# Performance work log

Hardware: AMD Instinct MI355X
Metric: run time of the kernel (lower is better)

## Reference

```python
import jax, jax.numpy as jnp
import numpy as np

N_NODES = 50000
N_EDGES = 800000
D_NODE = 128
D_EDGE = 128
D_HID = 128
D_OUT = 128


def setup_inputs() -> dict:
    key = jax.random.key(0)
    ks = jax.random.split(key, 6)
    d_in = 2 * D_NODE + D_EDGE  # 384
    return {
        "cell_attr": jax.random.normal(ks[0], (N_NODES, D_NODE), dtype=jnp.float32),
        "edge_attr": jax.random.normal(ks[1], (N_EDGES, D_EDGE), dtype=jnp.float32),
        "W1": jax.random.normal(ks[2], (d_in, D_HID), dtype=jnp.float32) * (1.0 / np.sqrt(d_in)),
        "b1": jnp.zeros((D_HID,), dtype=jnp.float32),
        "W2": jax.random.normal(ks[3], (D_HID, D_OUT), dtype=jnp.float32) * (1.0 / np.sqrt(D_HID)),
        "b2": jnp.zeros((D_OUT,), dtype=jnp.float32),
        "edge_index": jax.random.randint(ks[4], (2, N_EDGES), 0, N_NODES, dtype=jnp.int64) if jax.config.jax_enable_x64 else jax.random.randint(ks[4], (2, N_EDGES), 0, N_NODES, dtype=jnp.int32),
    }


def reference(cell_attr, edge_attr, W1, b1, W2, b2, edge_index):
    # Gather sender/receiver node features via edge_index: [E, d_node] each
    senders_attr = cell_attr[edge_index[0]]
    receivers_attr = cell_attr[edge_index[1]]
    # Concat -> [E, 2*d_node + d_edge]
    collected = jnp.concatenate([senders_attr, receivers_attr, edge_attr], axis=1)
    # MLP (custom_func): Linear -> ReLU -> Linear
    h = jax.nn.relu(collected @ W1 + b1)
    edge_attr_new = h @ W2 + b2
    return edge_attr_new
```

## Files before the change

### kernel.cpp

```cpp
#include <hip/hip_runtime.h>
#include <stdint.h>

#define D 128
#define K1 384
#define TM 128
#define LDA 136
#define N_EDGES 800000
#define N_NODES 50000

typedef __attribute__((ext_vector_type(8))) short short8;
typedef __attribute__((ext_vector_type(4))) float f32x4;

__device__ __forceinline__ unsigned int bf16_rne(float f) {
    unsigned int u = __builtin_bit_cast(unsigned int, f);
    return (u + 0x7FFFu + ((u >> 16) & 1u)) >> 16;
}

__global__ void prep_cell(const float* __restrict__ src, unsigned short* __restrict__ dst, int n4) {
    int i = blockIdx.x * blockDim.x + threadIdx.x;
    if (i >= n4) return;
    float4 v = ((const float4*)src)[i];
    ushort4 o;
    o.x = (unsigned short)bf16_rne(v.x);
    o.y = (unsigned short)bf16_rne(v.y);
    o.z = (unsigned short)bf16_rne(v.z);
    o.w = (unsigned short)bf16_rne(v.w);
    ((ushort4*)dst)[i] = o;
}

__global__ void prep_w(const float* __restrict__ W1, const float* __restrict__ W2,
                       unsigned short* __restrict__ W1T, unsigned short* __restrict__ W2T) {
    int id = blockIdx.x * blockDim.x + threadIdx.x;
    if (id < K1 * D) {
        int n = id & 127, k = id >> 7;
        W1T[n * K1 + k] = (unsigned short)bf16_rne(W1[id]);
    } else {
        int id2 = id - K1 * D;
        int n = id2 & 127, k = id2 >> 7;
        W2T[n * D + k] = (unsigned short)bf16_rne(W2[id2]);
    }
}

template <bool CELL_BF16>
__global__ __launch_bounds__(256, 2) void edge_mlp(
    const float* __restrict__ cell_f32,
    const unsigned short* __restrict__ cellb,
    const float* __restrict__ edge_attr,
    const unsigned short* __restrict__ W1T,
    const float* __restrict__ b1,
    const unsigned short* __restrict__ W2T,
    const float* __restrict__ b2,
    const int* __restrict__ sidx,
    const int* __restrict__ ridx,
    float* __restrict__ out)
{
    __shared__ __align__(16) unsigned short sA[TM * LDA];
    __shared__ __align__(16) unsigned short sB[D * LDA];
    __shared__ int   sIdx[2 * TM];
    __shared__ float sBias[2 * D];

    const int tid  = threadIdx.x;
    const int lane = tid & 63;
    const int wave = tid >> 6;
    const int e0   = blockIdx.x * TM;
    const int seg  = tid & 15;
    const int rb   = tid >> 4;

    if (tid < TM) sIdx[tid] = sidx[e0 + tid];
    else          sIdx[tid] = ridx[e0 + tid - TM];
    sBias[tid] = (tid < D) ? b1[tid] : b2[tid - D];

    const int l16  = lane & 15;
    const int quad = lane >> 4;

    f32x4 acc[2][8];
#pragma unroll
    for (int i = 0; i < 2; ++i)
#pragma unroll
        for (int j = 0; j < 8; ++j)
            acc[i][j] = (f32x4){0.f, 0.f, 0.f, 0.f};

    for (int c = 0; c < 3; ++c) {
        __syncthreads();

        if (c < 2) {
#pragma unroll
            for (int it = 0; it < 8; ++it) {
                int row = rb + it * 16;
                int node = sIdx[c * TM + row];
                if (CELL_BF16) {
                    uint4 v = *(const uint4*)(cellb + node * D + seg * 8);
                    *(uint4*)(&sA[row * LDA + seg * 8]) = v;
                } else {
                    const float* src = cell_f32 + (size_t)node * D + seg * 8;
                    float4 f0 = *(const float4*)(src);
                    float4 f1 = *(const float4*)(src + 4);
                    uint4 v;
                    v.x = bf16_rne(f0.x) | (bf16_rne(f0.y) << 16);
                    v.y = bf16_rne(f0.z) | (bf16_rne(f0.w) << 16);
                    v.z = bf16_rne(f1.x) | (bf16_rne(f1.y) << 16);
                    v.w = bf16_rne(f1.z) | (bf16_rne(f1.w) << 16);
                    *(uint4*)(&sA[row * LDA + seg * 8]) = v;
                }
            }
        } else {
#pragma unroll
            for (int it = 0; it < 8; ++it) {
                int row = rb + it * 16;
                const float* src = edge_attr + (size_t)(e0 + row) * D + seg * 8;
                float4 f0 = *(const float4*)(src);
                float4 f1 = *(const float4*)(src + 4);
                uint4 v;
                v.x = bf16_rne(f0.x) | (bf16_rne(f0.y) << 16);
                v.y = bf16_rne(f0.z) | (bf16_rne(f0.w) << 16);
                v.z = bf16_rne(f1.x) | (bf16_rne(f1.y) << 16);
                v.w = bf16_rne(f1.z) | (bf16_rne(f1.w) << 16);
                *(uint4*)(&sA[row * LDA + seg * 8]) = v;
            }
        }
#pragma unroll
        for (int it = 0; it < 8; ++it) {
            int row = rb + it * 16;
            uint4 v = *(const uint4*)(W1T + row * K1 + c * D + seg * 8);
            *(uint4*)(&sB[row * LDA + seg * 8]) = v;
        }
        __syncthreads();

#pragma unroll
        for (int kk = 0; kk < 4; ++kk) {
            const int ko = kk * 32 + quad * 8;
            short8 a0 = *(const short8*)(&sA[(wave * 32 + l16) * LDA + ko]);
            short8 a1 = *(const short8*)(&sA[(wave * 32 + 16 + l16) * LDA + ko]);
#pragma unroll
            for (int nt = 0; nt < 8; ++nt) {
                short8 b = *(const short8*)(&sB[(nt * 16 + l16) * LDA + ko]);
                acc[0][nt] = __builtin_amdgcn_mfma_f32_16x16x32_bf16(a0, b, acc[0][nt], 0, 0, 0);
                acc[1][nt] = __builtin_amdgcn_mfma_f32_16x16x32_bf16(a1, b, acc[1][nt], 0, 0, 0);
            }
        }
    }

#pragma unroll
    for (int mt = 0; mt < 2; ++mt) {
        const int mbase = wave * 32 + mt * 16 + quad * 4;
#pragma unroll
        for (int nt = 0; nt < 8; ++nt) {
            const int n = nt * 16 + l16;
            const float bias = sBias[n];
#pragma unroll
            for (int r = 0; r < 4; ++r) {
                float v = acc[mt][nt][r] + bias;
                v = v > 0.f ? v : 0.f;
                sA[(mbase + r) * LDA + n] = (unsigned short)bf16_rne(v);
            }
        }
    }
    __syncthreads();

#pragma unroll
    for (int it = 0; it < 8; ++it) {
        int row = rb + it * 16;
        uint4 v = *(const uint4*)(W2T + row * D + seg * 8);
        *(uint4*)(&sB[row * LDA + seg * 8]) = v;
    }
    __syncthreads();

    f32x4 acc2[2][8];
#pragma unroll
    for (int i = 0; i < 2; ++i)
#pragma unroll
        for (int j = 0; j < 8; ++j)
            acc2[i][j] = (f32x4){0.f, 0.f, 0.f, 0.f};

#pragma unroll
    for (int kk = 0; kk < 4; ++kk) {
        const int ko = kk * 32 + quad * 8;
        short8 a0 = *(const short8*)(&sA[(wave * 32 + l16) * LDA + ko]);
        short8 a1 = *(const short8*)(&sA[(wave * 32 + 16 + l16) * LDA + ko]);
#pragma unroll
        for (int nt = 0; nt < 8; ++nt) {
            short8 b = *(const short8*)(&sB[(nt * 16 + l16) * LDA + ko]);
            acc2[0][nt] = __builtin_amdgcn_mfma_f32_16x16x32_bf16(a0, b, acc2[0][nt], 0, 0, 0);
            acc2[1][nt] = __builtin_amdgcn_mfma_f32_16x16x32_bf16(a1, b, acc2[1][nt], 0, 0, 0);
        }
    }

#pragma unroll
    for (int mt = 0; mt < 2; ++mt) {
        const int mbase = wave * 32 + mt * 16 + quad * 4;
#pragma unroll
        for (int nt = 0; nt < 8; ++nt) {
            const int n = nt * 16 + l16;
            const float bias = sBias[D + n];
#pragma unroll
            for (int r = 0; r < 4; ++r) {
                out[(size_t)(e0 + mbase + r) * D + n] = acc2[mt][nt][r] + bias;
            }
        }
    }
}

extern "C" void kernel_launch(void* const* d_in, const int* in_sizes, int n_in,
                              void* d_out, int out_size, void* d_ws, size_t ws_size,
                              hipStream_t stream) {
    const float* cell = (const float*)d_in[0];
    const float* edge = (const float*)d_in[1];
    const float* W1   = (const float*)d_in[2];
    const float* b1   = (const float*)d_in[3];
    const float* W2   = (const float*)d_in[4];
    const float* b2   = (const float*)d_in[5];
    const int*   eidx = (const int*)d_in[6];

    const size_t cell_bytes = (size_t)N_NODES * D * 2;
    const size_t w1t_bytes  = (size_t)K1 * D * 2;
    const size_t w2t_bytes  = (size_t)D * D * 2;

    bool cell_in_ws = ws_size >= cell_bytes + w1t_bytes + w2t_bytes;
    unsigned short* cellb;
    unsigned short* W1T;
    if (cell_in_ws) {
        cellb = (unsigned short*)d_ws;
        W1T   = (unsigned short*)((char*)d_ws + cell_bytes);
    } else {
        cellb = nullptr;
        W1T   = (unsigned short*)d_ws;
    }
    unsigned short* W2T = W1T + K1 * D;

    if (cell_in_ws) {
        int n4 = N_NODES * D / 4;
        prep_cell<<<(n4 + 255) / 256, 256, 0, stream>>>(cell, cellb, n4);
    }
    prep_w<<<(K1 * D + D * D) / 256, 256, 0, stream>>>(W1, W2, W1T, W2T);

    const int* sidx = eidx;
    const int* ridx = eidx + N_EDGES;
    if (cell_in_ws) {
        edge_mlp<true><<<N_EDGES / TM, 256, 0, stream>>>(
            cell, cellb, edge, W1T, b1, W2T, b2, sidx, ridx, (float*)d_out);
    } else {
        edge_mlp<false><<<N_EDGES / TM, 256, 0, stream>>>(
            cell, cellb, edge, W1T, b1, W2T, b2, sidx, ridx, (float*)d_out);
    }
}
```

Baseline: 745.6 us.

## Load MLP operands straight into registers and keep only hidden tile in LDS

Rewrites the fused edge MLP so each wave owns a 64x64 output tile in a 2x2 wave grid. Weight fragments and gathered node and edge rows are loaded directly from global memory into MFMA registers, which removes the LDS staging and most barriers. The matmul is transposed (weights as A operand) so each lane's accumulator holds contiguous output columns, giving vectorized float4 stores. Only the hidden activations go through LDS, using an XOR-swizzled layout. The cost is much higher register pressure, which may lower occupancy or cause spills, and each wave now re-fetches weights from global/L2.

```diff
diff --git a/kernel.cpp b/kernel.cpp
--- a/kernel.cpp
+++ b/kernel.cpp
@@ -4,16 +4,19 @@
 #define D 128
 #define K1 384
 #define TM 128
-#define LDA 136
 #define N_EDGES 800000
 #define N_NODES 50000
 
 typedef __attribute__((ext_vector_type(8))) short short8;
 typedef __attribute__((ext_vector_type(4))) float f32x4;
-
-__device__ __forceinline__ unsigned int bf16_rne(float f) {
-    unsigned int u = __builtin_bit_cast(unsigned int, f);
+typedef unsigned int u32;
+
+__device__ __forceinline__ u32 bf16_rne(float f) {
+    u32 u = __builtin_bit_cast(u32, f);
     return (u + 0x7FFFu + ((u >> 16) & 1u)) >> 16;
+}
+__device__ __forceinline__ u32 pk2(float lo, float hi) {
+    return bf16_rne(lo) | (bf16_rne(hi) << 16);
 }
 
 __global__ void prep_cell(const float* __restrict__ src, unsigned short* __restrict__ dst, int n4) {
@@ -54,150 +57,163 @@
     const int* __restrict__ ridx,
     float* __restrict__ out)
 {
-    __shared__ __align__(16) unsigned short sA[TM * LDA];
-    __shared__ __align__(16) unsigned short sB[D * LDA];
-    __shared__ int   sIdx[2 * TM];
-    __shared__ float sBias[2 * D];
+    __shared__ __align__(16) unsigned short sH[TM * D];
 
     const int tid  = threadIdx.x;
     const int lane = tid & 63;
     const int wave = tid >> 6;
+    const int l16  = lane & 15;
+    const int q    = lane >> 4;
+    const int wm   = wave >> 1;
+    const int wn   = wave & 1;
     const int e0   = blockIdx.x * TM;
-    const int seg  = tid & 15;
-    const int rb   = tid >> 4;
-
-    if (tid < TM) sIdx[tid] = sidx[e0 + tid];
-    else          sIdx[tid] = ridx[e0 + tid - TM];
-    sBias[tid] = (tid < D) ? b1[tid] : b2[tid - D];
-
-    const int l16  = lane & 15;
-    const int quad = lane >> 4;
-
-    f32x4 acc[2][8];
-#pragma unroll
-    for (int i = 0; i < 2; ++i)
-#pragma unroll
-        for (int j = 0; j < 8; ++j)
-            acc[i][j] = (f32x4){0.f, 0.f, 0.f, 0.f};
-
-    for (int c = 0; c < 3; ++c) {
-        __syncthreads();
-
-        if (c < 2) {
-#pragma unroll
-            for (int it = 0; it < 8; ++it) {
-                int row = rb + it * 16;
-                int node = sIdx[c * TM + row];
-                if (CELL_BF16) {
-                    uint4 v = *(const uint4*)(cellb + node * D + seg * 8);
-                    *(uint4*)(&sA[row * LDA + seg * 8]) = v;
-                } else {
-                    const float* src = cell_f32 + (size_t)node * D + seg * 8;
-                    float4 f0 = *(const float4*)(src);
-                    float4 f1 = *(const float4*)(src + 4);
-                    uint4 v;
-                    v.x = bf16_rne(f0.x) | (bf16_rne(f0.y) << 16);
-                    v.y = bf16_rne(f0.z) | (bf16_rne(f0.w) << 16);
-                    v.z = bf16_rne(f1.x) | (bf16_rne(f1.y) << 16);
-                    v.w = bf16_rne(f1.z) | (bf16_rne(f1.w) << 16);
-                    *(uint4*)(&sA[row * LDA + seg * 8]) = v;
-                }
+    const int mrow = wm * 64 + l16;
+    const int ncol = wn * 64 + l16;
+
+    int idxs[4], idxr[4];
+#pragma unroll
+    for (int mt = 0; mt < 4; ++mt) {
+        idxs[mt] = sidx[e0 + mrow + mt * 16];
+        idxr[mt] = ridx[e0 + mrow + mt * 16];
+    }
+
+    short8 wf0[4][4];
+#pragma unroll
+    for (int nt = 0; nt < 4; ++nt) {
+        const unsigned short* wp = W1T + (size_t)(ncol + nt * 16) * K1 + 256 + q * 8;
+#pragma unroll
+        for (int kk = 0; kk < 4; ++kk) wf0[nt][kk] = *(const short8*)(wp + kk * 32);
+    }
+    short8 aE[4][4];
+#pragma unroll
+    for (int mt = 0; mt < 4; ++mt) {
+        const float* p = edge_attr + (size_t)(e0 + mrow + mt * 16) * D + q * 8;
+#pragma unroll
+        for (int kk = 0; kk < 4; ++kk) {
+            float4 f0 = *(const float4*)(p + kk * 32);
+            float4 f1 = *(const float4*)(p + kk * 32 + 4);
+            uint4 v = make_uint4(pk2(f0.x, f0.y), pk2(f0.z, f0.w), pk2(f1.x, f1.y), pk2(f1.z, f1.w));
+            aE[mt][kk] = __builtin_bit_cast(short8, v);
+        }
+    }
+
+    f32x4 acc[4][4];
+#pragma unroll
+    for (int i = 0; i < 4; ++i)
+#pragma unroll
+        for (int j = 0; j < 4; ++j) acc[i][j] = (f32x4){0.f, 0.f, 0.f, 0.f};
+
+    short8 aS[4][4], aR[4][4], wf1[4][4], wf2[4][4], w2f[4][4];
+
+#pragma unroll
+    for (int kk = 0; kk < 4; ++kk) {
+#pragma unroll
+        for (int nt = 0; nt < 4; ++nt)
+            wf1[nt][kk] = *(const short8*)(W1T + (size_t)(ncol + nt * 16) * K1 + kk * 32 + q * 8);
+#pragma unroll
+        for (int mt = 0; mt < 4; ++mt) {
+            if constexpr (CELL_BF16) {
+                aS[mt][kk] = *(const short8*)(cellb + (size_t)idxs[mt] * D + kk * 32 + q * 8);
+            } else {
+                const float* gp = cell_f32 + (size_t)idxs[mt] * D + kk * 32 + q * 8;
+                float4 f0 = *(const float4*)gp; float4 f1 = *(const float4*)(gp + 4);
+                uint4 v = make_uint4(pk2(f0.x, f0.y), pk2(f0.z, f0.w), pk2(f1.x, f1.y), pk2(f1.z, f1.w));
+                aS[mt][kk] = __builtin_bit_cast(short8, v);
             }
-        } else {
-#pragma unroll
-            for (int it = 0; it < 8; ++it) {
-                int row = rb + it * 16;
-                const float* src = edge_attr + (size_t)(e0 + row) * D + seg * 8;
-                float4 f0 = *(const float4*)(src);
-                float4 f1 = *(const float4*)(src + 4);
-                uint4 v;
-                v.x = bf16_rne(f0.x) | (bf16_rne(f0.y) << 16);
-                v.y = bf16_rne(f0.z) | (bf16_rne(f0.w) << 16);
-                v.z = bf16_rne(f1.x) | (bf16_rne(f1.y) << 16);
-                v.w = bf16_rne(f1.z) | (bf16_rne(f1.w) << 16);
-                *(uint4*)(&sA[row * LDA + seg * 8]) = v;
+        }
+#pragma unroll
+        for (int nt = 0; nt < 4; ++nt)
+#pragma unroll
+            for (int mt = 0; mt < 4; ++mt)
+                acc[nt][mt] = __builtin_amdgcn_mfma_f32_16x16x32_bf16(wf0[nt][kk], aE[mt][kk], acc[nt][mt], 0, 0, 0);
+    }
+
+#pragma unroll
+    for (int kk = 0; kk < 4; ++kk) {
+#pragma unroll
+        for (int nt = 0; nt < 4; ++nt)
+            wf2[nt][kk] = *(const short8*)(W1T + (size_t)(ncol + nt * 16) * K1 + 128 + kk * 32 + q * 8);
+#pragma unroll
+        for (int mt = 0; mt < 4; ++mt) {
+            if constexpr (CELL_BF16) {
+                aR[mt][kk] = *(const short8*)(cellb + (size_t)idxr[mt] * D + kk * 32 + q * 8);
+            } else {
+                const float* gp = cell_f32 + (size_t)idxr[mt] * D + kk * 32 + q * 8;
+                float4 f0 = *(const float4*)gp; float4 f1 = *(const float4*)(gp + 4);
+                uint4 v = make_uint4(pk2(f0.x, f0.y), pk2(f0.z, f0.w), pk2(f1.x, f1.y), pk2(f1.z, f1.w));
+                aR[mt][kk] = __builtin_bit_cast(short8, v);
             }
         }
 #pragma unroll
-        for (int it = 0; it < 8; ++it) {
-            int row = rb + it * 16;
-            uint4 v = *(const uint4*)(W1T + row * K1 + c * D + seg * 8);
-            *(uint4*)(&sB[row * LDA + seg * 8]) = v;
-        }
-        __syncthreads();
-
-#pragma unroll
-        for (int kk = 0; kk < 4; ++kk) {
-            const int ko = kk * 32 + quad * 8;
-            short8 a0 = *(const short8*)(&sA[(wave * 32 + l16) * LDA + ko]);
-            short8 a1 = *(const short8*)(&sA[(wave * 32 + 16 + l16) * LDA + ko]);
-#pragma unroll
-            for (int nt = 0; nt < 8; ++nt) {
-                short8 b = *(const short8*)(&sB[(nt * 16 + l16) * LDA + ko]);
-                acc[0][nt] = __builtin_amdgcn_mfma_f32_16x16x32_bf16(a0, b, acc[0][nt], 0, 0, 0);
-                acc[1][nt] = __builtin_amdgcn_mfma_f32_16x16x32_bf16(a1, b, acc[1][nt], 0, 0, 0);
-            }
-        }
-    }
-
-#pragma unroll
-    for (int mt = 0; mt < 2; ++mt) {
-        const int mbase = wave * 32 + mt * 16 + quad * 4;
-#pragma unroll
-        for (int nt = 0; nt < 8; ++nt) {
-            const int n = nt * 16 + l16;
-            const float bias = sBias[n];
-#pragma unroll
-            for (int r = 0; r < 4; ++r) {
-                float v = acc[mt][nt][r] + bias;
-                v = v > 0.f ? v : 0.f;
-                sA[(mbase + r) * LDA + n] = (unsigned short)bf16_rne(v);
-            }
-        }
-    }
+        for (int nt = 0; nt < 4; ++nt)
+#pragma unroll
+            for (int mt = 0; mt < 4; ++mt)
+                acc[nt][mt] = __builtin_amdgcn_mfma_f32_16x16x32_bf16(wf1[nt][kk], aS[mt][kk], acc[nt][mt], 0, 0, 0);
+    }
+
+    f32x4 b1v[4], b2v[4];
+#pragma unroll
+    for (int nt = 0; nt < 4; ++nt) {
+        b1v[nt] = *(const f32x4*)(b1 + wn * 64 + nt * 16 + q * 4);
+        b2v[nt] = *(const f32x4*)(b2 + wn * 64 + nt * 16 + q * 4);
+    }
+
+#pragma unroll
+    for (int kk = 0; kk < 4; ++kk) {
+#pragma unroll
+        for (int nt = 0; nt < 4; ++nt)
+            w2f[nt][kk] = *(const short8*)(W2T + (size_t)(ncol + nt * 16) * D + kk * 32 + q * 8);
+#pragma unroll
+        for (int nt = 0; nt < 4; ++nt)
+#pragma unroll
+            for (int mt = 0; mt < 4; ++mt)
+                acc[nt][mt] = __builtin_amdgcn_mfma_f32_16x16x32_bf16(wf2[nt][kk], aR[mt][kk], acc[nt][mt], 0, 0, 0);
+    }
+
+#pragma unroll
+    for (int nt = 0; nt < 4; ++nt)
+#pragma unroll
+        for (int mt = 0; mt < 4; ++mt) {
+            f32x4 v = acc[nt][mt] + b1v[nt];
+#pragma unroll
+            for (int r = 0; r < 4; ++r) v[r] = v[r] > 0.f ? v[r] : 0.f;
+            u32 lo = pk2(v[0], v[1]);
+            u32 hi = pk2(v[2], v[3]);
+            int M = wm * 64 + mt * 16 + l16;
+            int slot = (wn * 8 + nt * 2 + (q >> 1)) ^ (M & 7);
+            *(uint2*)((char*)sH + M * 256 + slot * 16 + (q & 1) * 8) = make_uint2(lo, hi);
+        }
     __syncthreads();
 
-#pragma unroll
-    for (int it = 0; it < 8; ++it) {
-        int row = rb + it * 16;
-        uint4 v = *(const uint4*)(W2T + row * D + seg * 8);
-        *(uint4*)(&sB[row * LDA + seg * 8]) = v;
-    }
-    __syncthreads();
-
-    f32x4 acc2[2][8];
-#pragma unroll
-    for (int i = 0; i < 2; ++i)
-#pragma unroll
-        for (int j = 0; j < 8; ++j)
-            acc2[i][j] = (f32x4){0.f, 0.f, 0.f, 0.f};
-
-#pragma unroll
-    for (int kk = 0; kk < 4; ++kk) {
-        const int ko = kk * 32 + quad * 8;
-        short8 a0 = *(const short8*)(&sA[(wave * 32 + l16) * LDA + ko]);
-        short8 a1 = *(const short8*)(&sA[(wave * 32 + 16 + l16) * LDA + ko]);
-#pragma unroll
-        for (int nt = 0; nt < 8; ++nt) {
-            short8 b = *(const short8*)(&sB[(nt * 16 + l16) * LDA + ko]);
-            acc2[0][nt] = __builtin_amdgcn_mfma_f32_16x16x32_bf16(a0, b, acc2[0][nt], 0, 0, 0);
-            acc2[1][nt] = __builtin_amdgcn_mfma_f32_16x16x32_bf16(a1, b, acc2[1][nt], 0, 0, 0);
-        }
-    }
-
-#pragma unroll
-    for (int mt = 0; mt < 2; ++mt) {
-        const int mbase = wave * 32 + mt * 16 + quad * 4;
-#pragma unroll
-        for (int nt = 0; nt < 8; ++nt) {
-            const int n = nt * 16 + l16;
-            const float bias = sBias[D + n];
-#pragma unroll
-            for (int r = 0; r < 4; ++r) {
-                out[(size_t)(e0 + mbase + r) * D + n] = acc2[mt][nt][r] + bias;
-            }
-        }
-    }
+    f32x4 acc2[4][4];
+#pragma unroll
+    for (int i = 0; i < 4; ++i)
+#pragma unroll
+        for (int j = 0; j < 4; ++j) acc2[i][j] = (f32x4){0.f, 0.f, 0.f, 0.f};
+
+#pragma unroll
+    for (int kk = 0; kk < 4; ++kk) {
+        short8 hf[4];
+#pragma unroll
+        for (int mt = 0; mt < 4; ++mt) {
+            int M = wm * 64 + mt * 16 + l16;
+            int slot = (kk * 4 + q) ^ (M & 7);
+            hf[mt] = *(const short8*)((const char*)sH + M * 256 + slot * 16);
+        }
+#pragma unroll
+        for (int nt = 0; nt < 4; ++nt)
+#pragma unroll
+            for (int mt = 0; mt < 4; ++mt)
+                acc2[nt][mt] = __builtin_amdgcn_mfma_f32_16x16x32_bf16(w2f[nt][kk], hf[mt], acc2[nt][mt], 0, 0, 0);
+    }
+
+#pragma unroll
+    for (int nt = 0; nt < 4; ++nt)
+#pragma unroll
+        for (int mt = 0; mt < 4; ++mt) {
+            f32x4 o = acc2[nt][mt] + b2v[nt];
+            *(f32x4*)(out + (size_t)(e0 + mrow + mt * 16) * D + wn * 64 + nt * 16 + q * 4) = o;
+        }
 }
 
 extern "C" void kernel_launch(void* const* d_in, const int* in_sizes, int n_in,
```

Measured after the change: 947.9 us. +27.1%, slower.
